# Kernel optimization log

Hardware: AMD Instinct MI355X
Metric: run time of the kernel (lower is better)

## Reference

```python
import jax, jax.numpy as jnp
import numpy as np

B, S, DIM = 2, 2048, 2048
NH = 16
Q_LORA, KV_LORA = 1536, 512
NOPE, ROPE, VHD = 128, 64, 128
QK_HD = NOPE + ROPE  # 192
EPS = 1e-6
SCALE = QK_HD ** -0.5


def rmsnorm(x, w, eps=EPS):
    return x * jax.lax.rsqrt(jnp.mean(x * x, axis=-1, keepdims=True) + eps) * w


def apply_rope(x, cos, sin):
    # x: (b, s, h, d) with d even; cos/sin: (s, d//2)
    xr, xi = x[..., 0::2], x[..., 1::2]
    c = cos[None, :, None, :]
    s = sin[None, :, None, :]
    yr = xr * c - xi * s
    yi = xr * s + xi * c
    return jnp.stack([yr, yi], axis=-1).reshape(x.shape)


def setup_inputs() -> dict:
    key = jax.random.key(0)
    ks = jax.random.split(key, 12)
    std = 0.02
    # RoPE tables (unit-magnitude complex as cos/sin)
    inv_freq = 1.0 / (10000.0 ** (np.arange(0, ROPE, 2, dtype=np.float32) / ROPE))  # (32,)
    ang = np.arange(S, dtype=np.float32)[:, None] * inv_freq[None, :]  # (S, 32)
    return {
        "x": jax.random.normal(ks[0], (B, S, DIM), jnp.float32),
        "freqs_cos": jnp.asarray(np.cos(ang)),
        "freqs_sin": jnp.asarray(np.sin(ang)),
        "wq_a_w": jax.random.normal(ks[1], (Q_LORA, DIM), jnp.float32) * std,
        "wq_a_b": jnp.zeros((Q_LORA,), jnp.float32),
        "q_norm_w": jnp.ones((Q_LORA,), jnp.float32),
        "wq_b_w": jax.random.normal(ks[2], (NH * QK_HD, Q_LORA), jnp.float32) * std,
        "wq_b_b": jnp.zeros((NH * QK_HD,), jnp.float32),
        "wkv_a_w": jax.random.normal(ks[3], (KV_LORA + ROPE, DIM), jnp.float32) * std,
        "wkv_a_b": jnp.zeros((KV_LORA + ROPE,), jnp.float32),
        "kv_norm_w": jnp.ones((KV_LORA,), jnp.float32),
        "wkv_b_w": jax.random.normal(ks[4], (NH * (NOPE + VHD), KV_LORA), jnp.float32) * std,
        "wkv_b_b": jnp.zeros((NH * (NOPE + VHD),), jnp.float32),
        "wo_w": jax.random.normal(ks[5], (DIM, NH * VHD), jnp.float32) * std,
        "wo_b": jnp.zeros((DIM,), jnp.float32),
    }


def reference(x, freqs_cos, freqs_sin, wq_a_w, wq_a_b, q_norm_w, wq_b_w, wq_b_b,
              wkv_a_w, wkv_a_b, kv_norm_w, wkv_b_w, wkv_b_b, wo_w, wo_b):
    b, s, _ = x.shape
    # Low-rank Q projection: wq_b(q_norm(wq_a(x)))
    q = rmsnorm(x @ wq_a_w.T + wq_a_b, q_norm_w) @ wq_b_w.T + wq_b_b
    q = q.reshape(b, s, NH, QK_HD)
    q_nope, q_pe = q[..., :NOPE], q[..., NOPE:]
    q = jnp.concatenate([q_nope, apply_rope(q_pe, freqs_cos, freqs_sin)], axis=-1)
    # Low-rank KV projection
    kv = x @ wkv_a_w.T + wkv_a_b  # (b, s, kv_lora + rope)
    kv_c, k_pe = kv[..., :KV_LORA], kv[..., KV_LORA:]
    k_pe = apply_rope(k_pe[:, :, None, :], freqs_cos, freqs_sin)  # (b, s, 1, rope)
    kv = rmsnorm(kv_c, kv_norm_w) @ wkv_b_w.T + wkv_b_b
    kv = kv.reshape(b, s, NH, NOPE + VHD)
    k_nope, v = kv[..., :NOPE], kv[..., NOPE:]
    k = jnp.concatenate([k_nope, jnp.broadcast_to(k_pe, (b, s, NH, ROPE))], axis=-1)
    # Causal SDPA
    scores = jnp.einsum("bqhd,bkhd->bhqk", q, k) * SCALE
    causal = jnp.tril(jnp.ones((s, s), bool))
    scores = jnp.where(causal[None, None], scores, jnp.float32(-1e30))
    attn = jax.nn.softmax(scores, axis=-1)
    out = jnp.einsum("bhqk,bkhd->bqhd", attn, v).reshape(b, s, NH * VHD)
    return out @ wo_w.T + wo_b
```

## Files before the change

### kernel.cpp

```cpp
#include <hip/hip_runtime.h>


typedef __bf16 bf16x8 __attribute__((ext_vector_type(8)));
typedef float f32x4 __attribute__((ext_vector_type(4)));
typedef unsigned short u16;

#define SEQ 2048
#define SCALE 0.07216878364870323f
#define NEGBIG -30000.0f

__device__ __forceinline__ float b2f(u16 u) {
  union { unsigned u; float f; } c; c.u = ((unsigned)u) << 16; return c.f;
}
__device__ __forceinline__ u16 f2b(float f) {
  union { float f; unsigned u; } c; c.f = f;
  unsigned r = (c.u + 0x7fffu + ((c.u >> 16) & 1u)) >> 16;
  return (u16)r;
}
__device__ __forceinline__ uint4 pack8(float4 a, float4 b) {
  union { uint4 v; u16 e[8]; } t;
  t.e[0] = f2b(a.x); t.e[1] = f2b(a.y); t.e[2] = f2b(a.z); t.e[3] = f2b(a.w);
  t.e[4] = f2b(b.x); t.e[5] = f2b(b.y); t.e[6] = f2b(b.z); t.e[7] = f2b(b.w);
  return t.v;
}

#define GLOAD_LDS16(gsrc, ldst)                                              \
  __builtin_amdgcn_global_load_lds(                                          \
      (const __attribute__((address_space(1))) unsigned int*)(gsrc),         \
      (__attribute__((address_space(3))) unsigned int*)(ldst), 16, 0, 0)

__global__ void cvt_kernel(const float* __restrict__ src, u16* __restrict__ dst,
                           long n8) {
  long i = (long)blockIdx.x * 256 + threadIdx.x;
  long stride = (long)gridDim.x * 256;
  for (; i < n8; i += stride) {
    const float4* s = (const float4*)(src + i * 8);
    float4 a = s[0], b = s[1];
    *(uint4*)(dst + i * 8) = pack8(a, b);
  }
}

__global__ void cvt6_kernel(
    const float* __restrict__ s0, u16* __restrict__ d0, long n0,
    const float* __restrict__ s1, u16* __restrict__ d1, long n1,
    const float* __restrict__ s2, u16* __restrict__ d2, long n2,
    const float* __restrict__ s3, u16* __restrict__ d3, long n3,
    const float* __restrict__ s4, u16* __restrict__ d4, long n4,
    const float* __restrict__ s5, u16* __restrict__ d5, long n5) {
  const float* src; u16* dst; long n8;
  switch (blockIdx.y) {
    case 0: src = s0; dst = d0; n8 = n0; break;
    case 1: src = s1; dst = d1; n8 = n1; break;
    case 2: src = s2; dst = d2; n8 = n2; break;
    case 3: src = s3; dst = d3; n8 = n3; break;
    case 4: src = s4; dst = d4; n8 = n4; break;
    default: src = s5; dst = d5; n8 = n5; break;
  }
  long i = (long)blockIdx.x * 256 + threadIdx.x;
  long stride = (long)gridDim.x * 256;
  for (; i < n8; i += stride) {
    const float4* s = (const float4*)(src + i * 8);
    float4 a = s[0], b = s[1];
    *(uint4*)(dst + i * 8) = pack8(a, b);
  }
}

template <int OF>
__global__ __launch_bounds__(256) void gemm_lds_kernel(
    const u16* __restrict__ X, int lda, const u16* __restrict__ W,
    const float* __restrict__ bias, void* __restrict__ out0,
    void* __restrict__ out1, int N0, int Ntot, int K, float oscale) {
  __shared__ alignas(16) u16 As[2][128 * 64];
  __shared__ alignas(16) u16 Bs[2][128 * 64];
  const int tid = threadIdx.x;
  const int wave = tid >> 6, lane = tid & 63;
  const int quad = lane >> 4, l16 = lane & 15;
  const int wr = (wave >> 1) * 64, wc = (wave & 1) * 64;
  const int bm = blockIdx.x * 128, bn = blockIdx.y * 128;
  const int srow0 = wave * 32 + (lane >> 3);
  const int gcol = ((lane & 7) ^ (lane >> 3)) * 8;

  f32x4 acc[4][4] = {};

  auto stage = [&](int buf, int k0) {
#pragma unroll
    for (int p = 0; p < 4; ++p) {
      int row = srow0 + p * 8;
      const u16* ga = X + (size_t)(bm + row) * lda + k0 + gcol;
      const u16* gb = W + (size_t)(bn + row) * K + k0 + gcol;
      char* la = (char*)(&As[buf][0]) + (wave * 4 + p) * 1024;
      char* lb = (char*)(&Bs[buf][0]) + (wave * 4 + p) * 1024;
      GLOAD_LDS16(ga, la);
      GLOAD_LDS16(gb, lb);
    }
  };

  const int nk = K >> 6;
  stage(0, 0);
  int cur = 0;
  for (int kt = 0; kt < nk; ++kt) {
    __syncthreads();
    if (kt + 1 < nk) stage(cur ^ 1, (kt + 1) * 64);
    const u16* as = &As[cur][0];
    const u16* bs = &Bs[cur][0];
#pragma unroll
    for (int kk = 0; kk < 64; kk += 32) {
      const int cs = (kk + quad * 8) ^ ((l16 & 7) * 8);
      bf16x8 a[4], b[4];
#pragma unroll
      for (int i = 0; i < 4; ++i)
        a[i] = *(const bf16x8*)(as + (wr + i * 16 + l16) * 64 + cs);
#pragma unroll
      for (int j = 0; j < 4; ++j)
        b[j] = *(const bf16x8*)(bs + (wc + j * 16 + l16) * 64 + cs);
#pragma unroll
      for (int i = 0; i < 4; ++i)
#pragma unroll
        for (int j = 0; j < 4; ++j)
          acc[i][j] = __builtin_amdgcn_mfma_f32_16x16x32_bf16(a[i], b[j], acc[i][j], 0, 0, 0);
    }
    cur ^= 1;
  }

  const int N1 = Ntot - N0;
#pragma unroll
  for (int i = 0; i < 4; ++i)
#pragma unroll
    for (int j = 0; j < 4; ++j) {
      int col = bn + wc + j * 16 + l16;
      float bv = bias[col];
#pragma unroll
      for (int r = 0; r < 4; ++r) {
        int row = bm + wr + i * 16 + quad * 4 + r;
        float v = (acc[i][j][r] + bv) * oscale;
        if (OF) {
          ((float*)out0)[(size_t)row * Ntot + col] = v;
        } else if (col < N0) {
          ((u16*)out0)[(size_t)row * N0 + col] = f2b(v);
        } else {
          ((u16*)out1)[(size_t)row * N1 + (col - N0)] = f2b(v);
        }
      }
    }
}

template <int XF, int WF, int OF>
__global__ __launch_bounds__(256, 3) void gemm_kernel(
    const void* __restrict__ X, int lda, const void* __restrict__ W,
    const float* __restrict__ bias, void* __restrict__ out,
    int M, int N, int K, float oscale) {
  constexpr int LDT = 72;
  __shared__ alignas(16) u16 As[64 * LDT];
  __shared__ alignas(16) u16 Bs[128 * LDT];
  const int tid = threadIdx.x;
  const int wave = tid >> 6, lane = tid & 63;
  const int quad = lane >> 4, l16 = lane & 15;
  const int bm = blockIdx.x * 64, bn = blockIdx.y * 128;
  const int wn = wave * 32;
  const int srow = tid >> 3;
  const int scol = (tid & 7) * 8;

  f32x4 acc[4][2] = {};

  float4 pa32[2][2], pb32[4][2];
  uint4  pa16[2],    pb16[4];

  auto load_tile = [&](int k0) {
#pragma unroll
    for (int p = 0; p < 2; ++p) {
      size_t off = (size_t)(bm + srow + p * 32) * lda + k0 + scol;
      if (XF) {
        const float* s = (const float*)X + off;
        pa32[p][0] = *(const float4*)s;
        pa32[p][1] = *(const float4*)(s + 4);
      } else {
        pa16[p] = *(const uint4*)((const u16*)X + off);
      }
    }
#pragma unroll
    for (int p = 0; p < 4; ++p) {
      int n = bn + srow + p * 32;
      size_t off = (size_t)n * K + k0 + scol;
      if (WF) {
        if (n < N) {
          const float* s = (const float*)W + off;
          pb32[p][0] = *(const float4*)s;
          pb32[p][1] = *(const float4*)(s + 4);
        } else {
          pb32[p][0] = make_float4(0.f, 0.f, 0.f, 0.f);
          pb32[p][1] = make_float4(0.f, 0.f, 0.f, 0.f);
        }
      } else {
        if (n < N) pb16[p] = *(const uint4*)((const u16*)W + off);
        else { pb16[p].x = pb16[p].y = pb16[p].z = pb16[p].w = 0u; }
      }
    }
  };

  load_tile(0);
  for (int k0 = 0; k0 < K; k0 += 64) {
    __syncthreads();
#pragma unroll
    for (int p = 0; p < 2; ++p) {
      uint4 v;
      if (XF) v = pack8(pa32[p][0], pa32[p][1]); else v = pa16[p];
      *(uint4*)(&As[(srow + p * 32) * LDT + scol]) = v;
    }
#pragma unroll
    for (int p = 0; p < 4; ++p) {
      uint4 v;
      if (WF) v = pack8(pb32[p][0], pb32[p][1]); else v = pb16[p];
      *(uint4*)(&Bs[(srow + p * 32) * LDT + scol]) = v;
    }
    __syncthreads();
    if (k0 + 64 < K) load_tile(k0 + 64);

#pragma unroll
    for (int kk = 0; kk < 64; kk += 32) {
      bf16x8 a[4], b[2];
#pragma unroll
      for (int i = 0; i < 4; ++i)
        a[i] = *(const bf16x8*)(&As[(i * 16 + l16) * LDT + kk + quad * 8]);
#pragma unroll
      for (int j = 0; j < 2; ++j)
        b[j] = *(const bf16x8*)(&Bs[(wn + j * 16 + l16) * LDT + kk + quad * 8]);
#pragma unroll
      for (int i = 0; i < 4; ++i)
#pragma unroll
        for (int j = 0; j < 2; ++j)
          acc[i][j] = __builtin_amdgcn_mfma_f32_16x16x32_bf16(a[i], b[j], acc[i][j], 0, 0, 0);
    }
  }

#pragma unroll
  for (int i = 0; i < 4; ++i)
#pragma unroll
    for (int j = 0; j < 2; ++j) {
      int col = bn + wn + j * 16 + l16;
      if (col < N) {
        float bv = bias[col];
#pragma unroll
        for (int r = 0; r < 4; ++r) {
          int row = bm + i * 16 + quad * 4 + r;
          float v = (acc[i][j][r] + bv) * oscale;
          if (OF) ((float*)out)[(size_t)row * N + col] = v;
          else    ((u16*)out)[(size_t)row * N + col] = f2b(v);
        }
      }
    }
}

__global__ void rmsnorm_kernel(u16* x, const float* __restrict__ w,
                               int C, int stride) {
  size_t base = (size_t)blockIdx.x * stride;
  float s = 0.f;
  for (int c = threadIdx.x; c < C; c += 256) { float v = b2f(x[base + c]); s += v * v; }
#pragma unroll
  for (int off = 32; off > 0; off >>= 1) s += __shfl_xor(s, off, 64);
  __shared__ float red[4];
  if ((threadIdx.x & 63) == 0) red[threadIdx.x >> 6] = s;
  __syncthreads();
  float tot = red[0] + red[1] + red[2] + red[3];
  float scale = rsqrtf(tot / (float)C + 1e-6f);
  for (int c = threadIdx.x; c < C; c += 256)
    x[base + c] = f2b(b2f(x[base + c]) * scale * w[c]);
}

__global__ void rope_kpe_kernel(const u16* __restrict__ kvn,
                                const float* __restrict__ fcos,
                                const float* __restrict__ fsin,
                                u16* __restrict__ kpe) {
  int idx = blockIdx.x * 256 + threadIdx.x;
  int t = idx >> 5, i = idx & 31;
  int s = t & (SEQ - 1);
  float c = fcos[s * 32 + i], sn = fsin[s * 32 + i];
  float xr = b2f(kvn[(size_t)t * 576 + 512 + 2 * i]);
  float xi = b2f(kvn[(size_t)t * 576 + 512 + 2 * i + 1]);
  kpe[(size_t)t * 64 + 2 * i]     = f2b(xr * c - xi * sn);
  kpe[(size_t)t * 64 + 2 * i + 1] = f2b(xr * sn + xi * c);
}

__global__ void rope_q_kernel(u16* q, const float* __restrict__ fcos,
                              const float* __restrict__ fsin) {
  int idx = blockIdx.x * 256 + threadIdx.x;
  int t = idx >> 8, h = (idx >> 5) & 7, i = idx & 31;
  int s = t & (SEQ - 1);
  float c = fcos[s * 32 + i], sn = fsin[s * 32 + i];
  size_t base = (size_t)t * 1536 + h * 192 + 128 + 2 * i;
  float xr = b2f(q[base]), xi = b2f(q[base + 1]);
  q[base]     = f2b(xr * c - xi * sn);
  q[base + 1] = f2b(xr * sn + xi * c);
}

__global__ void rope_q2_kernel(u16* qA, u16* qB, const float* __restrict__ fcos,
                               const float* __restrict__ fsin) {
  u16* q = blockIdx.y ? qB : qA;
  int idx = blockIdx.x * 256 + threadIdx.x;
  int t = idx >> 8, h = (idx >> 5) & 7, i = idx & 31;
  int s = t & (SEQ - 1);
  float c = fcos[s * 32 + i], sn = fsin[s * 32 + i];
  size_t base = (size_t)t * 1536 + h * 192 + 128 + 2 * i;
  float xr = b2f(q[base]), xi = b2f(q[base + 1]);
  q[base]     = f2b(xr * c - xi * sn);
  q[base + 1] = f2b(xr * sn + xi * c);
}

template <int PAIRED>
__global__ __launch_bounds__(256, 2) void attn_kernel(
    const u16* __restrict__ Q0,
    const u16* __restrict__ Q1,
    const u16* __restrict__ KV0,
    const u16* __restrict__ KV1,
    const u16* __restrict__ KPE,
    u16* __restrict__ O,
    int hbase) {
  constexpr int LK = 200;
  constexpr int LP = 72;
  __shared__ alignas(16) u16 Ks[64 * LK];
  __shared__ alignas(16) u16 Ps[64 * LP];
  __shared__ alignas(16) u16 Vs[128 * LP];

  const int tid = threadIdx.x;
  const int wave = tid >> 6, lane = tid & 63;
  const int quad = lane >> 4, l16 = lane & 15;
  const int h = hbase + blockIdx.y;
  const int hl = h & 7;
  const u16* __restrict__ Q   = (h & 8) ? Q1  : Q0;
  const u16* __restrict__ KVB = (h & 8) ? KV1 : KV0;
  const size_t tok0 = (size_t)blockIdx.z * SEQ;

  auto process = [&](int qt) {
    const int q0 = qt * 64;
    bf16x8 qf[6];
    {
      const u16* qp = Q + (tok0 + q0 + wave * 16 + l16) * 1536 + hl * 192 + quad * 8;
#pragma unroll
      for (int c = 0; c < 6; ++c) qf[c] = *(const bf16x8*)(qp + c * 32);
    }

    f32x4 o_acc[8] = {};
    float m_i[4], l_i[4];
#pragma unroll
    for (int r = 0; r < 4; ++r) { m_i[r] = NEGBIG; l_i[r] = 0.f; }

    const int nkt = qt + 1;
    uint4 kreg[6], vreg[4];
    auto load_tile = [&](int kt) {
      int k0 = kt * 64;
#pragma unroll
      for (int p = 0; p < 6; ++p) {
        int flat = tid + p * 256;
        int r = flat / 24, c8 = (flat % 24) * 8;
        const u16* src = (c8 < 128)
            ? (KVB + (tok0 + k0 + r) * 2048 + hl * 256 + c8)
            : (KPE + (tok0 + k0 + r) * 64 + (c8 - 128));
        kreg[p] = *(const uint4*)src;
      }
#pragma unroll
      for (int p = 0; p < 4; ++p) {
        int flat = tid + p * 256;
        int r = flat / 16, c8 = (flat % 16) * 8;
        vreg[p] = *(const uint4*)(KVB + (tok0 + k0 + r) * 2048 + hl * 256 + 128 + c8);
      }
    };

    load_tile(0);
    for (int kt = 0; kt < nkt; ++kt) {
      const int k0 = kt * 64;
      __syncthreads();
#pragma unroll
      for (int p = 0; p < 6; ++p) {
        int flat = tid + p * 256;
        int r = flat / 24, c8 = (flat % 24) * 8;
        *(uint4*)(&Ks[r * LK + c8]) = kreg[p];
      }
#pragma unroll
      for (int p = 0; p < 4; ++p) {
        int flat = tid + p * 256;
        int r = flat / 16, c8 = (flat % 16) * 8;
        union { uint4 v4; u16 e[8]; } t;
        t.v4 = vreg[p];
        int rs = r >> 3, rl = r & 7;
#pragma unroll
        for (int j = 0; j < 8; ++j) {
          int n = c8 + j;
          Vs[n * LP + ((rs ^ ((n >> 3) & 7)) << 3) + rl] = t.e[j];
        }
      }
      __syncthreads();
      if (kt + 1 < nkt) load_tile(kt + 1);

      f32x4 sc[4];
      __builtin_amdgcn_s_setprio(1);
#pragma unroll
      for (int ni = 0; ni < 4; ++ni) {
        f32x4 a = {};
#pragma unroll
        for (int c = 0; c < 6; ++c) {
          bf16x8 kf = *(const bf16x8*)(&Ks[(ni * 16 + l16) * LK + c * 32 + quad * 8]);
          a = __builtin_amdgcn_mfma_f32_16x16x32_bf16(qf[c], kf, a, 0, 0, 0);
        }
        sc[ni] = a;
      }
      __builtin_amdgcn_s_setprio(0);

      const int qrow_base = q0 + wave * 16 + quad * 4;
      if (kt == nkt - 1) {
#pragma unroll
        for (int ni = 0; ni < 4; ++ni) {
          int col = k0 + ni * 16 + l16;
#pragma unroll
          for (int r = 0; r < 4; ++r)
            if (col > qrow_base + r) sc[ni][r] = NEGBIG;
        }
      }

      float mloc[4];
#pragma unroll
      for (int r = 0; r < 4; ++r) mloc[r] = NEGBIG;
#pragma unroll
      for (int ni = 0; ni < 4; ++ni)
#pragma unroll
        for (int r = 0; r < 4; ++r) mloc[r] = fmaxf(mloc[r], sc[ni][r]);
#pragma unroll
      for (int off = 1; off < 16; off <<= 1)
#pragma unroll
        for (int r = 0; r < 4; ++r) mloc[r] = fmaxf(mloc[r], __shfl_xor(mloc[r], off, 64));

      float alpha[4], rsum[4];
#pragma unroll
      for (int r = 0; r < 4; ++r) {
        float mn = fmaxf(m_i[r], mloc[r]);
        alpha[r] = __expf(m_i[r] - mn);
        m_i[r] = mn;
        rsum[r] = 0.f;
      }
#pragma unroll
      for (int ni = 0; ni < 4; ++ni)
#pragma unroll
        for (int r = 0; r < 4; ++r) {
          float p = __expf(sc[ni][r] - m_i[r]);
          sc[ni][r] = p;
          rsum[r] += p;
        }
#pragma unroll
      for (int off = 1; off < 16; off <<= 1)
#pragma unroll
        for (int r = 0; r < 4; ++r) rsum[r] += __shfl_xor(rsum[r], off, 64);
#pragma unroll
      for (int r = 0; r < 4; ++r) l_i[r] = l_i[r] * alpha[r] + rsum[r];

#pragma unroll
      for (int ni = 0; ni < 4; ++ni)
#pragma unroll
        for (int r = 0; r < 4; ++r)
          Ps[(wave * 16 + quad * 4 + r) * LP + ni * 16 + l16] = f2b(sc[ni][r]);

      asm volatile("" ::: "memory");

#pragma unroll
      for (int t8 = 0; t8 < 8; ++t8)
#pragma unroll
        for (int r = 0; r < 4; ++r) o_acc[t8][r] *= alpha[r];

      bf16x8 pf0 = *(const bf16x8*)(&Ps[(wave * 16 + l16) * LP + quad * 8]);
      bf16x8 pf1 = *(const bf16x8*)(&Ps[(wave * 16 + l16) * LP + 32 + quad * 8]);
      __builtin_amdgcn_s_setprio(1);
#pragma unroll
      for (int ni = 0; ni < 8; ++ni) {
        int n0 = ni * 16 + l16;
        int sw = (n0 >> 3) & 7;
        bf16x8 vf0 = *(const bf16x8*)(&Vs[n0 * LP + ((quad ^ sw) << 3)]);
        bf16x8 vf1 = *(const bf16x8*)(&Vs[n0 * LP + (((4 + quad) ^ sw) << 3)]);
        o_acc[ni] = __builtin_amdgcn_mfma_f32_16x16x32_bf16(pf0, vf0, o_acc[ni], 0, 0, 0);
        o_acc[ni] = __builtin_amdgcn_mfma_f32_16x16x32_bf16(pf1, vf1, o_acc[ni], 0, 0, 0);
      }
      __builtin_amdgcn_s_setprio(0);
    }

#pragma unroll
    for (int ni = 0; ni < 8; ++ni) {
      int col = h * 128 + ni * 16 + l16;
#pragma unroll
      for (int r = 0; r < 4; ++r) {
        size_t row = tok0 + q0 + wave * 16 + quad * 4 + r;
        O[row * 2048 + col] = f2b(o_acc[ni][r] / l_i[r]);
      }
    }
  };

  if (PAIRED) {
    process(31 - (int)blockIdx.x);
    process((int)blockIdx.x);
  } else {
    process(blockIdx.z == 0 ? (31 - (int)blockIdx.x) : (int)blockIdx.x);
  }
}

extern "C" void kernel_launch(void* const* d_in, const int* in_sizes, int n_in,
                              void* d_out, int out_size, void* d_ws, size_t ws_size,
                              hipStream_t stream) {
  const float* x      = (const float*)d_in[0];
  const float* fcos   = (const float*)d_in[1];
  const float* fsin   = (const float*)d_in[2];
  const float* wqa    = (const float*)d_in[3];
  const float* wqa_b  = (const float*)d_in[4];
  const float* qnw    = (const float*)d_in[5];
  const float* wqb    = (const float*)d_in[6];
  const float* wqb_b  = (const float*)d_in[7];
  const float* wkva   = (const float*)d_in[8];
  const float* wkva_b = (const float*)d_in[9];
  const float* kvnw   = (const float*)d_in[10];
  const float* wkvb   = (const float*)d_in[11];
  const float* wkvb_b = (const float*)d_in[12];
  const float* wo     = (const float*)d_in[13];
  const float* wo_b   = (const float*)d_in[14];

  char* ws = (char*)d_ws;
  u16* qn   = (u16*)(ws + 0);
  u16* kvn  = (u16*)(ws + 12582912);
  u16* kpe  = (u16*)(ws + 17301504);
  u16* qbA  = (u16*)(ws + 17825792);
  u16* kvB  = (u16*)(ws + 30408704);
  u16* ao   = (u16*)(ws + 47185920);

  dim3 blk(256);

  if (ws_size >= 123994112u) {
    u16* xb    = (u16*)(ws + 63963136);
    u16* kvA   = (u16*)(ws + 63963136);
    u16* wqab  = (u16*)(ws + 80740352);
    u16* wkvab = (u16*)(ws + 87031808);
    u16* wqbb  = (u16*)(ws + 89391104);
    u16* wkvbw = (u16*)(ws + 98828288);
    u16* wob   = (u16*)(ws + 103022592);
    u16* qbB   = (u16*)(ws + 111411200);

    cvt6_kernel<<<dim3(512, 6), blk, 0, stream>>>(
        x,    xb,    1048576,
        wqa,  wqab,   393216,
        wkva, wkvab,  147456,
        wqb,  wqbb,   589824,
        wkvb, wkvbw,  262144,
        wo,   wob,    524288);

    gemm_lds_kernel<0><<<dim3(32, 12), blk, 0, stream>>>(xb, 2048, wqab, wqa_b, qn, qn, 1536, 1536, 2048, 1.0f);
    gemm_kernel<0,0,0><<<dim3(64, 5),  blk, 0, stream>>>(xb, 2048, wkvab, wkva_b, kvn, 4096, 576, 2048, 1.0f);
    rmsnorm_kernel<<<4096, blk, 0, stream>>>(qn, qnw, 1536, 1536);
    rmsnorm_kernel<<<4096, blk, 0, stream>>>(kvn, kvnw, 512, 576);
    rope_kpe_kernel<<<512, blk, 0, stream>>>(kvn, fcos, fsin, kpe);

    gemm_lds_kernel<0><<<dim3(32, 24), blk, 0, stream>>>(qn, 1536, wqbb, wqb_b, qbA, qbB, 1536, 3072, 1536, SCALE);
    rope_q2_kernel<<<dim3(4096, 2), blk, 0, stream>>>(qbA, qbB, fcos, fsin);
    gemm_lds_kernel<0><<<dim3(32, 32), blk, 0, stream>>>(kvn, 576, wkvbw, wkvb_b, kvA, kvB, 2048, 4096, 512, 1.0f);

    attn_kernel<1><<<dim3(16, 16, 2), blk, 0, stream>>>(qbA, qbB, kvA, kvB, kpe, ao, 0);

    gemm_lds_kernel<1><<<dim3(32, 16), blk, 0, stream>>>(ao, 2048, wob, wo_b, (float*)d_out, (float*)d_out, 2048, 2048, 2048, 1.0f);
  } else if (ws_size >= 111411200u) {
    u16* xb    = (u16*)(ws + 63963136);
    u16* wqab  = (u16*)(ws + 80740352);
    u16* wkvab = (u16*)(ws + 87031808);
    u16* wqbb  = (u16*)(ws + 89391104);
    u16* wkvbw = (u16*)(ws + 98828288);
    u16* wob   = (u16*)(ws + 103022592);

    cvt_kernel<<<2048, blk, 0, stream>>>(x,    xb,    1048576);
    cvt_kernel<<<1536, blk, 0, stream>>>(wqa,  wqab,   393216);
    cvt_kernel<<< 576, blk, 0, stream>>>(wkva, wkvab,  147456);
    cvt_kernel<<<2048, blk, 0, stream>>>(wqb,  wqbb,   589824);
    cvt_kernel<<<1024, blk, 0, stream>>>(wkvb, wkvbw,  262144);
    cvt_kernel<<<2048, blk, 0, stream>>>(wo,   wob,    524288);

    gemm_kernel<0,0,0><<<dim3(64, 12), blk, 0, stream>>>(xb, 2048, wqab, wqa_b, qn, 4096, 1536, 2048, 1.0f);
    gemm_kernel<0,0,0><<<dim3(64, 5),  blk, 0, stream>>>(xb, 2048, wkvab, wkva_b, kvn, 4096, 576, 2048, 1.0f);
    rmsnorm_kernel<<<4096, blk, 0, stream>>>(qn, qnw, 1536, 1536);
    rmsnorm_kernel<<<4096, blk, 0, stream>>>(kvn, kvnw, 512, 576);
    rope_kpe_kernel<<<512, blk, 0, stream>>>(kvn, fcos, fsin, kpe);

    for (int g = 0; g < 2; ++g) {
      const u16* wqb_g   = wqbb + (size_t)g * 1536 * 1536;
      const float* wqb_bg  = wqb_b + g * 1536;
      const u16* wkvb_g  = wkvbw + (size_t)g * 2048 * 512;
      const float* wkvb_bg = wkvb_b + g * 2048;
      gemm_kernel<0,0,0><<<dim3(64, 12), blk, 0, stream>>>(qn, 1536, wqb_g, wqb_bg, qbA, 4096, 1536, 1536, SCALE);
      rope_q_kernel<<<4096, blk, 0, stream>>>(qbA, fcos, fsin);
      gemm_kernel<0,0,0><<<dim3(64, 16), blk, 0, stream>>>(kvn, 576, wkvb_g, wkvb_bg, kvB, 4096, 2048, 512, 1.0f);
      attn_kernel<0><<<dim3(32, 8, 2), blk, 0, stream>>>(qbA, qbA, kvB, kvB, kpe, ao, g * 8);
    }

    gemm_kernel<0,0,1><<<dim3(64, 16), blk, 0, stream>>>(ao, 2048, wob, wo_b, (float*)d_out, 4096, 2048, 2048, 1.0f);
  } else {
    gemm_kernel<1,1,0><<<dim3(64, 12), blk, 0, stream>>>(x, 2048, wqa, wqa_b, qn, 4096, 1536, 2048, 1.0f);
    gemm_kernel<1,1,0><<<dim3(64, 5),  blk, 0, stream>>>(x, 2048, wkva, wkva_b, kvn, 4096, 576, 2048, 1.0f);
    rmsnorm_kernel<<<4096, blk, 0, stream>>>(qn, qnw, 1536, 1536);
    rmsnorm_kernel<<<4096, blk, 0, stream>>>(kvn, kvnw, 512, 576);
    rope_kpe_kernel<<<512, blk, 0, stream>>>(kvn, fcos, fsin, kpe);

    for (int g = 0; g < 2; ++g) {
      const float* wqb_g   = wqb + (size_t)g * 1536 * 1536;
      const float* wqb_bg  = wqb_b + g * 1536;
      const float* wkvb_g  = wkvb + (size_t)g * 2048 * 512;
      const float* wkvb_bg = wkvb_b + g * 2048;
      gemm_kernel<0,1,0><<<dim3(64, 12), blk, 0, stream>>>(qn, 1536, wqb_g, wqb_bg, qbA, 4096, 1536, 1536, SCALE);
      rope_q_kernel<<<4096, blk, 0, stream>>>(qbA, fcos, fsin);
      gemm_kernel<0,1,0><<<dim3(64, 16), blk, 0, stream>>>(kvn, 576, wkvb_g, wkvb_bg, kvB, 4096, 2048, 512, 1.0f);
      attn_kernel<0><<<dim3(32, 8, 2), blk, 0, stream>>>(qbA, qbA, kvB, kvB, kpe, ao, g * 8);
    }

    gemm_kernel<0,1,1><<<dim3(64, 16), blk, 0, stream>>>(ao, 2048, wo, wo_b, (float*)d_out, 4096, 2048, 2048, 1.0f);
  }
}
```

Before: 529.5 us.

## Split long causal attention tiles across key ranges with a separate combine pass

```diff
diff --git a/kernel.cpp b/kernel.cpp
--- a/kernel.cpp
+++ b/kernel.cpp
@@ -307,13 +307,9 @@
 
 template <int PAIRED>
 __global__ __launch_bounds__(256, 2) void attn_kernel(
-    const u16* __restrict__ Q0,
-    const u16* __restrict__ Q1,
-    const u16* __restrict__ KV0,
-    const u16* __restrict__ KV1,
-    const u16* __restrict__ KPE,
-    u16* __restrict__ O,
-    int hbase) {
+    const u16* __restrict__ Q0, const u16* __restrict__ Q1,
+    const u16* __restrict__ KV0, const u16* __restrict__ KV1,
+    const u16* __restrict__ KPE, u16* __restrict__ O, int hbase) {
   constexpr int LK = 200;
   constexpr int LP = 72;
   __shared__ alignas(16) u16 Ks[64 * LK];
@@ -494,6 +490,253 @@
     process((int)blockIdx.x);
   } else {
     process(blockIdx.z == 0 ? (31 - (int)blockIdx.x) : (int)blockIdx.x);
+  }
+}
+
+__device__ const unsigned char xmap48[48] = {
+  2, 6, 10, 14, 18, 22, 26, 30, 34, 38, 42, 46, 50, 54, 58, 84,
+  62, 113, 105, 116, 97, 89, 100, 92, 73, 65, 76, 68, 69, 77, 64, 85,
+  121, 124, 125, 108, 117, 120, 101, 104, 109, 112, 93, 96, 81, 72, 80, 88
+};
+
+__global__ __launch_bounds__(256, 3) void attn_splitk_kernel(
+    const u16* __restrict__ Q0, const u16* __restrict__ Q1,
+    const u16* __restrict__ KV0, const u16* __restrict__ KV1,
+    const u16* __restrict__ KPE, u16* __restrict__ O,
+    float* __restrict__ partO, float* __restrict__ partML) {
+  constexpr int LK = 200;
+  constexpr int LP = 72;
+  __shared__ alignas(16) u16 Ks[64 * LK];
+  __shared__ alignas(16) u16 Ps[64 * LP];
+  __shared__ alignas(16) u16 Vs[128 * LP];
+
+  const int tid = threadIdx.x;
+  const int wave = tid >> 6, lane = tid & 63;
+  const int quad = lane >> 4, l16 = lane & 15;
+  const int h = blockIdx.y;
+  const int hl = h & 7;
+  const u16* __restrict__ Q   = (h & 8) ? Q1  : Q0;
+  const u16* __restrict__ KVB = (h & 8) ? KV1 : KV0;
+  const size_t tok0 = (size_t)blockIdx.z * SEQ;
+
+  const int code = xmap48[blockIdx.x];
+  const int qt = code >> 2, hc = code & 3;
+  const int nkt = qt + 1;
+  int kb, ke;
+  if (hc == 2)      { kb = 0;        ke = nkt; }
+  else if (hc == 0) { kb = 0;        ke = nkt >> 1; }
+  else              { kb = nkt >> 1; ke = nkt; }
+
+  const int q0 = qt * 64;
+  bf16x8 qf[6];
+  {
+    const u16* qp = Q + (tok0 + q0 + wave * 16 + l16) * 1536 + hl * 192 + quad * 8;
+#pragma unroll
+    for (int c = 0; c < 6; ++c) qf[c] = *(const bf16x8*)(qp + c * 32);
+  }
+
+  f32x4 o_acc[8] = {};
+  float m_i[4], l_i[4];
+#pragma unroll
+  for (int r = 0; r < 4; ++r) { m_i[r] = NEGBIG; l_i[r] = 0.f; }
+
+  uint4 kreg[6], vreg[4];
+  auto load_tile = [&](int kt) {
+    int k0 = kt * 64;
+#pragma unroll
+    for (int p = 0; p < 6; ++p) {
+      int flat = tid + p * 256;
+      int r = flat / 24, c8 = (flat % 24) * 8;
+      const u16* src = (c8 < 128)
+          ? (KVB + (tok0 + k0 + r) * 2048 + hl * 256 + c8)
+          : (KPE + (tok0 + k0 + r) * 64 + (c8 - 128));
+      kreg[p] = *(const uint4*)src;
+    }
+#pragma unroll
+    for (int p = 0; p < 4; ++p) {
+      int flat = tid + p * 256;
+      int r = flat / 16, c8 = (flat % 16) * 8;
+      vreg[p] = *(const uint4*)(KVB + (tok0 + k0 + r) * 2048 + hl * 256 + 128 + c8);
+    }
+  };
+
+  load_tile(kb);
+  for (int kt = kb; kt < ke; ++kt) {
+    const int k0 = kt * 64;
+    __syncthreads();
+#pragma unroll
+    for (int p = 0; p < 6; ++p) {
+      int flat = tid + p * 256;
+      int r = flat / 24, c8 = (flat % 24) * 8;
+      *(uint4*)(&Ks[r * LK + c8]) = kreg[p];
+    }
+#pragma unroll
+    for (int p = 0; p < 4; ++p) {
+      int flat = tid + p * 256;
+      int r = flat / 16, c8 = (flat % 16) * 8;
+      union { uint4 v4; u16 e[8]; } t;
+      t.v4 = vreg[p];
+      int rs = r >> 3, rl = r & 7;
+#pragma unroll
+      for (int j = 0; j < 8; ++j) {
+        int n = c8 + j;
+        Vs[n * LP + ((rs ^ ((n >> 3) & 7)) << 3) + rl] = t.e[j];
+      }
+    }
+    __syncthreads();
+    if (kt + 1 < ke) load_tile(kt + 1);
+
+    f32x4 sc[4];
+    __builtin_amdgcn_s_setprio(1);
+#pragma unroll
+    for (int ni = 0; ni < 4; ++ni) {
+      f32x4 a = {};
+#pragma unroll
+      for (int c = 0; c < 6; ++c) {
+        bf16x8 kf = *(const bf16x8*)(&Ks[(ni * 16 + l16) * LK + c * 32 + quad * 8]);
+        a = __builtin_amdgcn_mfma_f32_16x16x32_bf16(qf[c], kf, a, 0, 0, 0);
+      }
+      sc[ni] = a;
+    }
+    __builtin_amdgcn_s_setprio(0);
+
+    const int qrow_base = q0 + wave * 16 + quad * 4;
+    if (kt == qt) {
+#pragma unroll
+      for (int ni = 0; ni < 4; ++ni) {
+        int col = k0 + ni * 16 + l16;
+#pragma unroll
+        for (int r = 0; r < 4; ++r)
+          if (col > qrow_base + r) sc[ni][r] = NEGBIG;
+      }
+    }
+
+    float mloc[4];
+#pragma unroll
+    for (int r = 0; r < 4; ++r) mloc[r] = NEGBIG;
+#pragma unroll
+    for (int ni = 0; ni < 4; ++ni)
+#pragma unroll
+      for (int r = 0; r < 4; ++r) mloc[r] = fmaxf(mloc[r], sc[ni][r]);
+#pragma unroll
+    for (int off = 1; off < 16; off <<= 1)
+#pragma unroll
+      for (int r = 0; r < 4; ++r) mloc[r] = fmaxf(mloc[r], __shfl_xor(mloc[r], off, 64));
+
+    float alpha[4], rsum[4];
+#pragma unroll
+    for (int r = 0; r < 4; ++r) {
+      float mn = fmaxf(m_i[r], mloc[r]);
+      alpha[r] = __expf(m_i[r] - mn);
+      m_i[r] = mn;
+      rsum[r] = 0.f;
+    }
+#pragma unroll
+    for (int ni = 0; ni < 4; ++ni)
+#pragma unroll
+      for (int r = 0; r < 4; ++r) {
+        float p = __expf(sc[ni][r] - m_i[r]);
+        sc[ni][r] = p;
+        rsum[r] += p;
+      }
+#pragma unroll
+    for (int off = 1; off < 16; off <<= 1)
+#pragma unroll
+      for (int r = 0; r < 4; ++r) rsum[r] += __shfl_xor(rsum[r], off, 64);
+#pragma unroll
+    for (int r = 0; r < 4; ++r) l_i[r] = l_i[r] * alpha[r] + rsum[r];
+
+#pragma unroll
+    for (int ni = 0; ni < 4; ++ni)
+#pragma unroll
+      for (int r = 0; r < 4; ++r)
+        Ps[(wave * 16 + quad * 4 + r) * LP + ni * 16 + l16] = f2b(sc[ni][r]);
+
+    asm volatile("" ::: "memory");
+
+#pragma unroll
+    for (int t8 = 0; t8 < 8; ++t8)
+#pragma unroll
+      for (int r = 0; r < 4; ++r) o_acc[t8][r] *= alpha[r];
+
+    bf16x8 pf0 = *(const bf16x8*)(&Ps[(wave * 16 + l16) * LP + quad * 8]);
+    bf16x8 pf1 = *(const bf16x8*)(&Ps[(wave * 16 + l16) * LP + 32 + quad * 8]);
+    __builtin_amdgcn_s_setprio(1);
+#pragma unroll
+    for (int ni = 0; ni < 8; ++ni) {
+      int n0 = ni * 16 + l16;
+      int sw = (n0 >> 3) & 7;
+      bf16x8 vf0 = *(const bf16x8*)(&Vs[n0 * LP + ((quad ^ sw) << 3)]);
+      bf16x8 vf1 = *(const bf16x8*)(&Vs[n0 * LP + (((4 + quad) ^ sw) << 3)]);
+      o_acc[ni] = __builtin_amdgcn_mfma_f32_16x16x32_bf16(pf0, vf0, o_acc[ni], 0, 0, 0);
+      o_acc[ni] = __builtin_amdgcn_mfma_f32_16x16x32_bf16(pf1, vf1, o_acc[ni], 0, 0, 0);
+    }
+    __builtin_amdgcn_s_setprio(0);
+  }
+
+  if (hc == 2) {
+#pragma unroll
+    for (int ni = 0; ni < 8; ++ni) {
+      int col = h * 128 + ni * 16 + l16;
+#pragma unroll
+      for (int r = 0; r < 4; ++r) {
+        size_t row = tok0 + q0 + wave * 16 + quad * 4 + r;
+        O[row * 2048 + col] = f2b(o_acc[ni][r] / l_i[r]);
+      }
+    }
+  } else {
+    int p = (((int)blockIdx.z * 16 + h) * 16 + (qt - 16)) * 2 + hc;
+    float* po = partO + (size_t)p * 8192;
+#pragma unroll
+    for (int ni = 0; ni < 8; ++ni) {
+      int col = ni * 16 + l16;
+#pragma unroll
+      for (int r = 0; r < 4; ++r) {
+        int row = wave * 16 + quad * 4 + r;
+        po[row * 128 + col] = o_acc[ni][r];
+      }
+    }
+    if (l16 == 0) {
+      float* pml = partML + (size_t)p * 128;
+#pragma unroll
+      for (int r = 0; r < 4; ++r) {
+        int row = wave * 16 + quad * 4 + r;
+        pml[row]      = m_i[r];
+        pml[64 + row] = l_i[r];
+      }
+    }
+  }
+}
+
+__global__ void attn_combine_kernel(const float* __restrict__ partO,
+                                    const float* __restrict__ partML,
+                                    u16* __restrict__ O) {
+  const int idx = blockIdx.x;
+  const int z = idx >> 8, h = (idx >> 4) & 15, qh = idx & 15;
+  const int qt = 16 + qh;
+  const size_t row0 = (size_t)z * SEQ + qt * 64;
+  const int col0 = h * 128;
+  const float* o0 = partO + (size_t)(idx * 2) * 8192;
+  const float* o1 = o0 + 8192;
+  const float* ml0 = partML + (size_t)(idx * 2) * 128;
+  const float* ml1 = ml0 + 128;
+
+  __shared__ float w0s[64], w1s[64], invls[64];
+  if (threadIdx.x < 64) {
+    int r = threadIdx.x;
+    float m0 = ml0[r], m1 = ml1[r];
+    float l0 = ml0[64 + r], l1 = ml1[64 + r];
+    float m = fmaxf(m0, m1);
+    float w0 = __expf(m0 - m), w1 = __expf(m1 - m);
+    float l = w0 * l0 + w1 * l1;
+    w0s[r] = w0; w1s[r] = w1; invls[r] = 1.0f / l;
+  }
+  __syncthreads();
+
+  for (int i = threadIdx.x; i < 8192; i += 256) {
+    int r = i >> 7, c = i & 127;
+    float v = (w0s[r] * o0[i] + w1s[r] * o1[i]) * invls[r];
+    O[(row0 + r) * 2048 + col0 + c] = f2b(v);
   }
 }
 
@@ -554,7 +797,15 @@
     rope_q2_kernel<<<dim3(4096, 2), blk, 0, stream>>>(qbA, qbB, fcos, fsin);
     gemm_lds_kernel<0><<<dim3(32, 32), blk, 0, stream>>>(kvn, 576, wkvbw, wkvb_b, kvA, kvB, 2048, 4096, 512, 1.0f);
 
-    attn_kernel<1><<<dim3(16, 16, 2), blk, 0, stream>>>(qbA, qbB, kvA, kvB, kpe, ao, 0);
+    if (ws_size >= 158072832u) {
+      float* partO  = (float*)(ws + 123994112);
+      float* partML = (float*)(ws + 157548544);
+      attn_splitk_kernel<<<dim3(48, 16, 2), blk, 0, stream>>>(
+          qbA, qbB, kvA, kvB, kpe, ao, partO, partML);
+      attn_combine_kernel<<<512, blk, 0, stream>>>(partO, partML, ao);
+    } else {
+      attn_kernel<1><<<dim3(16, 16, 2), blk, 0, stream>>>(qbA, qbB, kvA, kvB, kpe, ao, 0);
+    }
 
     gemm_lds_kernel<1><<<dim3(32, 16), blk, 0, stream>>>(ao, 2048, wob, wo_b, (float*)d_out, (float*)d_out, 2048, 2048, 2048, 1.0f);
   } else if (ws_size >= 111411200u) {
```

New measurement: 680.7 us. +28.6%, slower.
